# Optimization experiments

Measured on AMD Instinct MI355X. Metric: run time of the kernel, lower is better.

## Reference

```python
import jax, jax.numpy as jnp
import numpy as np

NUM_HEADS = 16
NEG_INF = -9000000000000000.0


def setup_inputs() -> dict:
    key = jax.random.key(0)
    ks = jax.random.split(key, 4)
    B, S, D = 2, 2048, 1024
    x = jax.random.normal(ks[0], (B, S, D), dtype=jnp.float32)
    mask = jax.random.randint(ks[1], (1, 1, S, S), 0, 2, dtype=jnp.int32)
    # xavier-uniform-ish init scaled down for stability
    w_qkv = jax.random.normal(ks[2], (3 * D, D), dtype=jnp.float32) * (1.0 / np.sqrt(D))
    b_qkv = jnp.zeros((3 * D,), dtype=jnp.float32)
    w_o = jax.random.normal(ks[3], (D, D), dtype=jnp.float32) * (1.0 / np.sqrt(D))
    b_o = jnp.zeros((D,), dtype=jnp.float32)
    return {"x": x, "mask": mask, "w_qkv": w_qkv, "b_qkv": b_qkv, "w_o": w_o, "b_o": b_o}


def reference(x, mask, w_qkv, b_qkv, w_o, b_o):
    B, S, D = x.shape
    H = NUM_HEADS
    hd = D // H
    # qkv projection: torch Linear is x @ W.T + b
    qkv = x @ w_qkv.T + b_qkv                      # [B, S, 3D]
    qkv = qkv.reshape(B, S, H, 3 * hd).transpose(0, 2, 1, 3)  # [B, H, S, 3hd]
    q, k, v = jnp.split(qkv, 3, axis=-1)           # each [B, H, S, hd]
    scale = 1.0 / np.sqrt(hd).astype(np.float32)
    logits = jnp.einsum("bhqd,bhkd->bhqk", q, k) * scale  # [B, H, S, S]
    logits = jnp.where(mask == 0, NEG_INF, logits)
    attn = jax.nn.softmax(logits, axis=-1)
    ctx = jnp.einsum("bhqk,bhkd->bhqd", attn, v)   # [B, H, S, hd]
    ctx = ctx.transpose(0, 2, 1, 3).reshape(B, S, D)
    return ctx @ w_o.T + b_o
```

## Files before the change

kernel.cpp:

```cpp
#include <hip/hip_runtime.h>

typedef __attribute__((ext_vector_type(8))) short short8;
typedef __attribute__((ext_vector_type(4))) float f32x4;

#define MFMA16(a, b, c) __builtin_amdgcn_mfma_f32_16x16x32_bf16(a, b, c, 0, 0, 0)

#define BATCH 2
#define SEQ 2048
#define DMODEL 1024
#define NHEADS 16
#define HDIM 64
#define MROWS (BATCH * SEQ)
#define N_QKV (3 * DMODEL)

#define QSCALE 0.1803368801111184f

#define GLDS16(gp, lp)                                                       \
  __builtin_amdgcn_global_load_lds(                                          \
      (const __attribute__((address_space(1))) void*)(gp),                   \
      (__attribute__((address_space(3))) void*)(lp), 16, 0, 0)

#define CFENCE() asm volatile("" ::: "memory")

static __device__ __forceinline__ unsigned short f2bf(float f) {
  unsigned int u = __float_as_uint(f);
  u = (u + 0x7fff + ((u >> 16) & 1)) >> 16;
  return (unsigned short)u;
}

static __device__ __forceinline__ unsigned int pk2bf(float lo, float hi) {
  unsigned int r;
  asm("v_cvt_pk_bf16_f32 %0, %1, %2" : "=v"(r) : "v"(lo), "v"(hi));
  return r;
}

static __device__ __forceinline__ float fexp2(float x) {
  float r;
  asm("v_exp_f32 %0, %1" : "=v"(r) : "v"(x));
  return r;
}

__global__ void prep_kernel(const int* __restrict__ mask,
                            unsigned int* __restrict__ bits,
                            const float* __restrict__ a, unsigned short* __restrict__ oa,
                            int na4, const float* __restrict__ b,
                            unsigned short* __restrict__ ob, int nb4,
                            const float* __restrict__ c,
                            unsigned short* __restrict__ oc, int nc4) {
  if (blockIdx.x < (SEQ * SEQ) / 256) {
    int i = blockIdx.x * 256 + threadIdx.x;
    unsigned long long bl = __ballot(mask[i] != 0);
    if ((threadIdx.x & 63) == 0)
      ((unsigned long long*)bits)[i >> 6] = bl;
    return;
  }
  int j = (blockIdx.x - (SEQ * SEQ) / 256) * 256 + threadIdx.x;
  const float* src;
  unsigned short* dst;
  if (j < na4) {
    src = a; dst = oa;
  } else if ((j -= na4) < nb4) {
    src = b; dst = ob;
  } else if ((j -= nb4) < nc4) {
    src = c; dst = oc;
  } else
    return;
  f32x4 v = ((const f32x4*)src)[j];
  ushort4 o;
  o.x = f2bf(v[0]); o.y = f2bf(v[1]); o.z = f2bf(v[2]); o.w = f2bf(v[3]);
  ((ushort4*)dst)[j] = o;
}

template <int EPI, int BM>
__global__ __launch_bounds__(256, 4) void gemm_bt(
    const unsigned short* __restrict__ A, const unsigned short* __restrict__ Bm,
    const float* __restrict__ bias, int Kdim, int Ndim,
    unsigned short* __restrict__ qb, unsigned short* __restrict__ kb,
    unsigned short* __restrict__ vtb, float* __restrict__ Cout) {
  constexpr int WM = (BM == 128) ? 64 : 32;
  constexpr int NI = WM / 16;
  __shared__ __align__(16) unsigned short lA[2][BM * 32];
  __shared__ __align__(16) unsigned short lB[2][128 * 32];

  int t = threadIdx.x;
  int nwg = gridDim.x * gridDim.y;
  int lin = blockIdx.y * gridDim.x + blockIdx.x;
  int swb = (lin & 7) * (nwg >> 3) + (lin >> 3);
  int m0 = (swb / gridDim.x) * BM, n0 = (swb % gridDim.x) * 128;

  int w = t >> 6, lane = t & 63, quad = lane >> 4, l16 = lane & 15;
  int wm = (w >> 1) * WM, wn = (w & 1) * 64;

  f32x4 acc[NI][4];
#pragma unroll
  for (int i = 0; i < NI; ++i)
#pragma unroll
    for (int j = 0; j < 4; ++j) acc[i][j] = (f32x4){0.f, 0.f, 0.f, 0.f};

  int nK = Kdim >> 5;

#define GSTAGE(buf, kk)                                                      \
  do {                                                                       \
    _Pragma("unroll")                                                        \
    for (int c = 0; c < BM / 64; ++c) {                                      \
      int id = t + c * 256;                                                  \
      int row = id >> 2;                                                     \
      int gc = ((id & 3) ^ (row & 3)) << 3; \
      GLDS16(&A[(size_t)(m0 + row) * Kdim + ((kk) << 5) + gc],               \
             (char*)lA[buf] + (id & ~63) * 16);                              \
    }                                                                        \
    _Pragma("unroll")                                                        \
    for (int c = 0; c < 2; ++c) {                                            \
      int id = t + c * 256;                                                  \
      int row = id >> 2;                                                     \
      int gc = ((id & 3) ^ (row & 3)) << 3;                                  \
      GLDS16(&Bm[(size_t)(n0 + row) * Kdim + ((kk) << 5) + gc],              \
             (char*)lB[buf] + (id & ~63) * 16);                              \
    }                                                                        \
  } while (0)

  GSTAGE(0, 0);
  for (int kk = 0; kk < nK; ++kk) {
    int cur = kk & 1;
    if (kk + 1 < nK) {
      GSTAGE(cur ^ 1, kk + 1);
      if (BM == 128)
        asm volatile("s_waitcnt vmcnt(4)" ::: "memory");
      else
        asm volatile("s_waitcnt vmcnt(3)" ::: "memory");
    } else {
      asm volatile("s_waitcnt vmcnt(0)" ::: "memory");
    }
    __builtin_amdgcn_s_barrier();
    CFENCE();
    __builtin_amdgcn_sched_barrier(0);

    short8 af[NI], bfr[4];
    int rswz = (l16 & 3) << 4;
#pragma unroll
    for (int i = 0; i < NI; ++i)
      af[i] = *(const short8*)((const char*)&lA[cur][(wm + i * 16 + l16) * 32] +
                               ((quad * 16) ^ rswz));
#pragma unroll
    for (int j = 0; j < 4; ++j)
      bfr[j] = *(const short8*)((const char*)&lB[cur][(wn + j * 16 + l16) * 32] +
                                ((quad * 16) ^ rswz));
#pragma unroll
    for (int i = 0; i < NI; ++i)
#pragma unroll
      for (int j = 0; j < 4; ++j) acc[i][j] = MFMA16(af[i], bfr[j], acc[i][j]);

    asm volatile("s_waitcnt lgkmcnt(0)" ::: "memory");
    __builtin_amdgcn_s_barrier();
    CFENCE();
  }

#pragma unroll
  for (int j = 0; j < 4; ++j) {
    int n = n0 + wn + j * 16 + l16;
    float bs = bias[n];
#pragma unroll
    for (int i = 0; i < NI; ++i) {
#pragma unroll
      for (int r = 0; r < 4; ++r) {
        int m = m0 + wm + i * 16 + quad * 4 + r;
        float v = acc[i][j][r] + bs;
        if (EPI == 0) {
          int b = m >> 11, s = m & 2047;
          int h = n / 192, rr = n % 192;
          int bh = (b << 4) + h;
          if (rr < 64)
            qb[((size_t)bh * SEQ + s) * HDIM + rr] = f2bf(v * QSCALE);
          else if (rr < 128)
            kb[((size_t)bh * SEQ + s) * HDIM + (rr - 64)] = f2bf(v);
          else
            vtb[((size_t)bh * HDIM + (rr - 128)) * SEQ + s] = f2bf(v);
        } else {
          Cout[(size_t)m * Ndim + n] = v;
        }
      }
    }
  }
}

__global__ __launch_bounds__(256, 2) void attn_kernel(
    const unsigned short* __restrict__ qbuf, const unsigned short* __restrict__ kbuf,
    const unsigned short* __restrict__ vtbuf, const unsigned int* __restrict__ mbits,
    unsigned short* __restrict__ ctx) {
  __shared__ __align__(16) unsigned short lK[2][64 * 64];
  __shared__ __align__(16) unsigned short lV[2][64 * 64];
  __shared__ __align__(16) unsigned short lP[128 * 64];

  int lin = blockIdx.y * gridDim.x + blockIdx.x;
  int slin = (lin & 7) * 64 + (lin >> 3);
  int qt = slin & 15, bh = slin >> 4;
  int q0 = qt * 128;
  const unsigned short* Q = qbuf + (size_t)bh * SEQ * HDIM;
  const unsigned short* K = kbuf + (size_t)bh * SEQ * HDIM;
  const unsigned short* VT = vtbuf + (size_t)bh * HDIM * SEQ;

  int t = threadIdx.x;
  int w = t >> 6, lane = t & 63, quad = lane >> 4, l16 = lane & 15;
  int swz = (l16 & 7) << 4;

  int qr0 = q0 + w * 32 + l16;
  short8 qf[2][2];
#pragma unroll
  for (int mt = 0; mt < 2; ++mt)
#pragma unroll
    for (int kh = 0; kh < 2; ++kh)
      qf[mt][kh] =
          *(const short8*)&Q[(size_t)(qr0 + mt * 16) * HDIM + kh * 32 + quad * 8];

  const short one = (short)0x3F80;
  short8 ones = {one, one, one, one, one, one, one, one};

  f32x4 o[2][4];
#pragma unroll
  for (int mt = 0; mt < 2; ++mt)
#pragma unroll
    for (int jt = 0; jt < 4; ++jt) o[mt][jt] = (f32x4){0.f, 0.f, 0.f, 0.f};
  f32x4 li4[2];
  li4[0] = (f32x4){0.f, 0.f, 0.f, 0.f};
  li4[1] = (f32x4){0.f, 0.f, 0.f, 0.f};

  int scol = ((lane & 7) ^ (lane >> 3)) << 3;
  const unsigned short* gK = K + (size_t)(w * 8 + (lane >> 3)) * HDIM + scol;
  const unsigned short* gV = VT + (size_t)(w * 8 + (lane >> 3)) * SEQ + scol;

#define STAGE_KV(buf)                                            \
  do {                                                           \
    GLDS16(gK, &lK[buf][(w * 8) * 64]);                          \
    GLDS16(gK + 32 * HDIM, &lK[buf][(32 + w * 8) * 64]);         \
    GLDS16(gV, &lV[buf][(w * 8) * 64]);                          \
    GLDS16(gV + 32 * SEQ, &lV[buf][(32 + w * 8) * 64]);          \
  } while (0)

  STAGE_KV(0);
  gK += 64 * HDIM;
  gV += 64;

  const unsigned int* mrow0 = mbits + (size_t)qr0 * 64;
  const unsigned int* mrow1 = mbits + (size_t)(qr0 + 16) * 64;
  unsigned short* lPr0 = &lP[(w * 32 + l16) * 64];
  unsigned short* lPr1 = &lP[(w * 32 + 16 + l16) * 64];

  for (int it = 0; it < SEQ / 64; ++it) {
    __syncthreads();
    if (it + 1 < SEQ / 64) {
      STAGE_KV((it + 1) & 1);
      gK += 64 * HDIM;
      gV += 64;
    }
    const unsigned short* cK = lK[it & 1];
    const unsigned short* cV = lV[it & 1];

    uint2 mw0 = *(const uint2*)&mrow0[it * 2];
    uint2 mw1 = *(const uint2*)&mrow1[it * 2];

    f32x4 s[2][4];
    __builtin_amdgcn_s_setprio(1);
#pragma unroll
    for (int j = 0; j < 4; ++j) {
      const char* kr = (const char*)&cK[(j * 16 + l16) * 64];
      short8 ka = *(const short8*)(kr + ((quad * 16) ^ swz));
      short8 kc = *(const short8*)(kr + ((64 + quad * 16) ^ swz));
#pragma unroll
      for (int mt = 0; mt < 2; ++mt) {
        f32x4 z = (f32x4){0.f, 0.f, 0.f, 0.f};
        z = MFMA16(ka, qf[mt][0], z);
        z = MFMA16(kc, qf[mt][1], z);
        s[mt][j] = z;
      }
    }
    __builtin_amdgcn_s_setprio(0);

#pragma unroll
    for (int mt = 0; mt < 2; ++mt) {
      unsigned int ma = (mt ? mw1.x : mw0.x) >> (quad * 4);
      unsigned int mb = (mt ? mw1.y : mw0.y) >> (quad * 4);
#pragma unroll
      for (int j = 0; j < 4; ++j) {
        unsigned int sel = (j < 2) ? ma : mb;
        int sh = (j & 1) << 4;
#pragma unroll
        for (int r = 0; r < 4; ++r) {
          float v = (sel & (1u << (sh + r))) ? s[mt][j][r] : -1e30f;
          s[mt][j][r] = fexp2(v);
        }
      }
    }

#pragma unroll
    for (int j = 0; j < 4; ++j) {
      uint2 u0, u1;
      u0.x = pk2bf(s[0][j][0], s[0][j][1]);
      u0.y = pk2bf(s[0][j][2], s[0][j][3]);
      u1.x = pk2bf(s[1][j][0], s[1][j][1]);
      u1.y = pk2bf(s[1][j][2], s[1][j][3]);
      *(uint2*)((char*)lPr0 + ((j * 32 + quad * 8) ^ swz)) = u0;
      *(uint2*)((char*)lPr1 + ((j * 32 + quad * 8) ^ swz)) = u1;
    }

    __builtin_amdgcn_s_setprio(1);
#pragma unroll
    for (int kh = 0; kh < 2; ++kh) {
      short8 pf0 = *(const short8*)((const char*)lPr0 + ((kh * 64 + quad * 16) ^ swz));
      short8 pf1 = *(const short8*)((const char*)lPr1 + ((kh * 64 + quad * 16) ^ swz));
      li4[0] = MFMA16(ones, pf0, li4[0]);
      li4[1] = MFMA16(ones, pf1, li4[1]);
#pragma unroll
      for (int jt = 0; jt < 4; ++jt) {
        const char* vr = (const char*)&cV[(jt * 16 + l16) * 64];
        short8 vf = *(const short8*)(vr + ((kh * 64 + quad * 16) ^ swz));
        o[0][jt] = MFMA16(vf, pf0, o[0][jt]);
        o[1][jt] = MFMA16(vf, pf1, o[1][jt]);
      }
    }
    __builtin_amdgcn_s_setprio(0);
  }

  int b = bh >> 4, h = bh & 15;
#pragma unroll
  for (int mt = 0; mt < 2; ++mt) {
    float inv = 1.0f / li4[mt][0];
    unsigned short* crow =
        ctx + ((size_t)(b * SEQ + qr0 + mt * 16)) * DMODEL + h * HDIM;
#pragma unroll
    for (int jt = 0; jt < 4; ++jt) {
      uint2 u;
      u.x = pk2bf(o[mt][jt][0] * inv, o[mt][jt][1] * inv);
      u.y = pk2bf(o[mt][jt][2] * inv, o[mt][jt][3] * inv);
      *(uint2*)&crow[jt * 16 + quad * 4] = u;
    }
  }
}

extern "C" void kernel_launch(void* const* d_in, const int* in_sizes, int n_in,
                              void* d_out, int out_size, void* d_ws, size_t ws_size,
                              hipStream_t stream) {
  const float* x = (const float*)d_in[0];
  const int* mask = (const int*)d_in[1];
  const float* w_qkv = (const float*)d_in[2];
  const float* b_qkv = (const float*)d_in[3];
  const float* w_o = (const float*)d_in[4];
  const float* b_o = (const float*)d_in[5];
  float* out = (float*)d_out;

  char* ws = (char*)d_ws;
  unsigned short* xb = (unsigned short*)(ws);
  unsigned short* wqkvb = (unsigned short*)(ws + (8ull << 20));
  unsigned short* wob = (unsigned short*)(ws + (14ull << 20));
  unsigned short* qb = (unsigned short*)(ws + (16ull << 20));
  unsigned short* kb = (unsigned short*)(ws + (24ull << 20));
  unsigned short* vtb = (unsigned short*)(ws + (32ull << 20));
  unsigned short* ctx = (unsigned short*)(ws + (40ull << 20));
  unsigned int* mbits = (unsigned int*)(ws + (48ull << 20));

  const int na4 = (MROWS * DMODEL) / 4;
  const int nb4 = (N_QKV * DMODEL) / 4;
  const int nc4 = (DMODEL * DMODEL) / 4;
  const int nmask = (SEQ * SEQ) / 256;
  const int ncvt = (na4 + nb4 + nc4 + 255) / 256;
  prep_kernel<<<nmask + ncvt, 256, 0, stream>>>(mask, mbits, x, xb, na4,
                                                w_qkv, wqkvb, nb4, w_o, wob, nc4);

  gemm_bt<0, 128><<<dim3(N_QKV / 128, MROWS / 128), 256, 0, stream>>>(
      xb, wqkvb, b_qkv, DMODEL, N_QKV, qb, kb, vtb, nullptr);

  attn_kernel<<<dim3(SEQ / 128, BATCH * NHEADS), 256, 0, stream>>>(
      qb, kb, vtb, mbits, ctx);

  gemm_bt<1, 64><<<dim3(DMODEL / 128, MROWS / 64), 256, 0, stream>>>(
      ctx, wob, b_o, DMODEL, DMODEL, nullptr, nullptr, nullptr, out);
}
```

Measured before the change: 216.9 us.

## Halve attention block size, vectorize V-transpose epilogue stores, prefetch mask bits

The attention kernel now uses 128-thread blocks covering 64 query rows instead of 256 threads over 128 rows. That doubles the grid, and each wave stages twice as many K/V rows per tile. The QKV GEMM epilogue hoists the head/column math and writes the transposed V rows as one 4-element vector store instead of four scalar stores. Mask words for the next iteration are loaded one step ahead to hide their latency. Smaller blocks add grid parallelism and cut LDS per block, but each K/V tile is now loaded by more blocks, so K/V global traffic rises.

```diff
diff --git a/kernel.cpp b/kernel.cpp
--- a/kernel.cpp
+++ b/kernel.cpp
@@ -159,42 +159,52 @@
   for (int j = 0; j < 4; ++j) {
     int n = n0 + wn + j * 16 + l16;
     float bs = bias[n];
+    int h = n / 192, rr = n % 192;
 #pragma unroll
     for (int i = 0; i < NI; ++i) {
-#pragma unroll
-      for (int r = 0; r < 4; ++r) {
-        int m = m0 + wm + i * 16 + quad * 4 + r;
-        float v = acc[i][j][r] + bs;
-        if (EPI == 0) {
-          int b = m >> 11, s = m & 2047;
-          int h = n / 192, rr = n % 192;
-          int bh = (b << 4) + h;
-          if (rr < 64)
-            qb[((size_t)bh * SEQ + s) * HDIM + rr] = f2bf(v * QSCALE);
-          else if (rr < 128)
-            kb[((size_t)bh * SEQ + s) * HDIM + (rr - 64)] = f2bf(v);
-          else
-            vtb[((size_t)bh * HDIM + (rr - 128)) * SEQ + s] = f2bf(v);
+      int mb_ = m0 + wm + i * 16 + quad * 4;
+      if (EPI == 0) {
+        int b = mb_ >> 11, s = mb_ & 2047;
+        int bh = (b << 4) + h;
+        if (rr < 64) {
+#pragma unroll
+          for (int r = 0; r < 4; ++r)
+            qb[((size_t)bh * SEQ + s + r) * HDIM + rr] =
+                f2bf((acc[i][j][r] + bs) * QSCALE);
+        } else if (rr < 128) {
+#pragma unroll
+          for (int r = 0; r < 4; ++r)
+            kb[((size_t)bh * SEQ + s + r) * HDIM + (rr - 64)] =
+                f2bf(acc[i][j][r] + bs);
         } else {
-          Cout[(size_t)m * Ndim + n] = v;
+          ushort4 u;
+          u.x = f2bf(acc[i][j][0] + bs);
+          u.y = f2bf(acc[i][j][1] + bs);
+          u.z = f2bf(acc[i][j][2] + bs);
+          u.w = f2bf(acc[i][j][3] + bs);
+          *(ushort4*)&vtb[((size_t)bh * HDIM + (rr - 128)) * SEQ + s] = u;
         }
+      } else {
+#pragma unroll
+        for (int r = 0; r < 4; ++r)
+          Cout[(size_t)(mb_ + r) * Ndim + n] = acc[i][j][r] + bs;
       }
     }
   }
 }
 
-__global__ __launch_bounds__(256, 2) void attn_kernel(
+__global__ __launch_bounds__(128, 2) void attn_kernel(
     const unsigned short* __restrict__ qbuf, const unsigned short* __restrict__ kbuf,
     const unsigned short* __restrict__ vtbuf, const unsigned int* __restrict__ mbits,
     unsigned short* __restrict__ ctx) {
   __shared__ __align__(16) unsigned short lK[2][64 * 64];
   __shared__ __align__(16) unsigned short lV[2][64 * 64];
-  __shared__ __align__(16) unsigned short lP[128 * 64];
+  __shared__ __align__(16) unsigned short lP[64 * 64];
 
   int lin = blockIdx.y * gridDim.x + blockIdx.x;
-  int slin = (lin & 7) * 64 + (lin >> 3);
-  int qt = slin & 15, bh = slin >> 4;
-  int q0 = qt * 128;
+  int slin = (lin & 7) * 128 + (lin >> 3);
+  int qt = slin & 31, bh = slin >> 5;
+  int q0 = qt * 64;
   const unsigned short* Q = qbuf + (size_t)bh * SEQ * HDIM;
   const unsigned short* K = kbuf + (size_t)bh * SEQ * HDIM;
   const unsigned short* VT = vtbuf + (size_t)bh * HDIM * SEQ;
@@ -225,15 +235,19 @@
   li4[1] = (f32x4){0.f, 0.f, 0.f, 0.f};
 
   int scol = ((lane & 7) ^ (lane >> 3)) << 3;
-  const unsigned short* gK = K + (size_t)(w * 8 + (lane >> 3)) * HDIM + scol;
-  const unsigned short* gV = VT + (size_t)(w * 8 + (lane >> 3)) * SEQ + scol;
+  const unsigned short* gK = K + (size_t)(w * 16 + (lane >> 3)) * HDIM + scol;
+  const unsigned short* gV = VT + (size_t)(w * 16 + (lane >> 3)) * SEQ + scol;
 
 #define STAGE_KV(buf)                                            \
   do {                                                           \
-    GLDS16(gK, &lK[buf][(w * 8) * 64]);                          \
-    GLDS16(gK + 32 * HDIM, &lK[buf][(32 + w * 8) * 64]);         \
-    GLDS16(gV, &lV[buf][(w * 8) * 64]);                          \
-    GLDS16(gV + 32 * SEQ, &lV[buf][(32 + w * 8) * 64]);          \
+    GLDS16(gK, &lK[buf][(w * 16) * 64]);                         \
+    GLDS16(gK + 8 * HDIM, &lK[buf][(w * 16 + 8) * 64]);          \
+    GLDS16(gK + 32 * HDIM, &lK[buf][(w * 16 + 32) * 64]);        \
+    GLDS16(gK + 40 * HDIM, &lK[buf][(w * 16 + 40) * 64]);        \
+    GLDS16(gV, &lV[buf][(w * 16) * 64]);                         \
+    GLDS16(gV + 8 * SEQ, &lV[buf][(w * 16 + 8) * 64]);           \
+    GLDS16(gV + 32 * SEQ, &lV[buf][(w * 16 + 32) * 64]);         \
+    GLDS16(gV + 40 * SEQ, &lV[buf][(w * 16 + 40) * 64]);         \
   } while (0)
 
   STAGE_KV(0);
@@ -245,18 +259,21 @@
   unsigned short* lPr0 = &lP[(w * 32 + l16) * 64];
   unsigned short* lPr1 = &lP[(w * 32 + 16 + l16) * 64];
 
+  uint2 mw0 = *(const uint2*)&mrow0[0];
+  uint2 mw1 = *(const uint2*)&mrow1[0];
+
   for (int it = 0; it < SEQ / 64; ++it) {
     __syncthreads();
+    uint2 nmw0, nmw1;
     if (it + 1 < SEQ / 64) {
       STAGE_KV((it + 1) & 1);
       gK += 64 * HDIM;
       gV += 64;
+      nmw0 = *(const uint2*)&mrow0[(it + 1) * 2];
+      nmw1 = *(const uint2*)&mrow1[(it + 1) * 2];
     }
     const unsigned short* cK = lK[it & 1];
     const unsigned short* cV = lV[it & 1];
-
-    uint2 mw0 = *(const uint2*)&mrow0[it * 2];
-    uint2 mw1 = *(const uint2*)&mrow1[it * 2];
 
     f32x4 s[2][4];
     __builtin_amdgcn_s_setprio(1);
@@ -290,6 +307,8 @@
         }
       }
     }
+    mw0 = nmw0;
+    mw1 = nmw1;
 
 #pragma unroll
     for (int j = 0; j < 4; ++j) {
@@ -368,7 +387,7 @@
   gemm_bt<0, 128><<<dim3(N_QKV / 128, MROWS / 128), 256, 0, stream>>>(
       xb, wqkvb, b_qkv, DMODEL, N_QKV, qb, kb, vtb, nullptr);
 
-  attn_kernel<<<dim3(SEQ / 128, BATCH * NHEADS), 256, 0, stream>>>(
+  attn_kernel<<<dim3(SEQ / 64, BATCH * NHEADS), 128, 0, stream>>>(
       qb, kb, vtb, mbits, ctx);
 
   gemm_bt<1, 64><<<dim3(DMODEL / 128, MROWS / 64), 256, 0, stream>>>(
```

Result: no change. 215.7 us (-0.6%).

## Triple-buffer GEMM global-to-LDS pipeline and vectorize V-transpose epilogue stores

Applied to the files above, without the earlier changes.

The GEMM mainloop goes from two LDS stages to three, issuing loads two K-steps ahead with adjusted vmcnt waits, to hide more global latency. Launch bounds drop from 4 to 3 waves per SIMD to fit the larger LDS footprint. The epilogue hoists per-column head math out of the inner loop and writes the transposed V output as 8-byte ushort4 stores instead of four scalar stores. The extra stage raises LDS use per block, which may lower occupancy.

```diff
diff --git a/kernel.cpp b/kernel.cpp
--- a/kernel.cpp
+++ b/kernel.cpp
@@ -72,15 +72,15 @@
 }
 
 template <int EPI, int BM>
-__global__ __launch_bounds__(256, 4) void gemm_bt(
+__global__ __launch_bounds__(256, 3) void gemm_bt(
     const unsigned short* __restrict__ A, const unsigned short* __restrict__ Bm,
     const float* __restrict__ bias, int Kdim, int Ndim,
     unsigned short* __restrict__ qb, unsigned short* __restrict__ kb,
     unsigned short* __restrict__ vtb, float* __restrict__ Cout) {
   constexpr int WM = (BM == 128) ? 64 : 32;
   constexpr int NI = WM / 16;
-  __shared__ __align__(16) unsigned short lA[2][BM * 32];
-  __shared__ __align__(16) unsigned short lB[2][128 * 32];
+  __shared__ __align__(16) unsigned short lA[3][BM * 32];
+  __shared__ __align__(16) unsigned short lB[3][128 * 32];
 
   int t = threadIdx.x;
   int nwg = gridDim.x * gridDim.y;
@@ -120,10 +120,18 @@
   } while (0)
 
   GSTAGE(0, 0);
+  GSTAGE(1, 1);
+  int stage = 2;
   for (int kk = 0; kk < nK; ++kk) {
-    int cur = kk & 1;
-    if (kk + 1 < nK) {
-      GSTAGE(cur ^ 1, kk + 1);
+    int cur = kk % 3;
+    if (kk + 2 < nK) {
+      GSTAGE(stage, kk + 2);
+      stage = (stage + 1) % 3;
+      if (BM == 128)
+        asm volatile("s_waitcnt vmcnt(8)" ::: "memory");
+      else
+        asm volatile("s_waitcnt vmcnt(6)" ::: "memory");
+    } else if (kk + 1 < nK) {
       if (BM == 128)
         asm volatile("s_waitcnt vmcnt(4)" ::: "memory");
       else
@@ -159,25 +167,35 @@
   for (int j = 0; j < 4; ++j) {
     int n = n0 + wn + j * 16 + l16;
     float bs = bias[n];
+    int h = n / 192, rr = n % 192;
 #pragma unroll
     for (int i = 0; i < NI; ++i) {
-#pragma unroll
-      for (int r = 0; r < 4; ++r) {
-        int m = m0 + wm + i * 16 + quad * 4 + r;
-        float v = acc[i][j][r] + bs;
-        if (EPI == 0) {
-          int b = m >> 11, s = m & 2047;
-          int h = n / 192, rr = n % 192;
-          int bh = (b << 4) + h;
-          if (rr < 64)
-            qb[((size_t)bh * SEQ + s) * HDIM + rr] = f2bf(v * QSCALE);
-          else if (rr < 128)
-            kb[((size_t)bh * SEQ + s) * HDIM + (rr - 64)] = f2bf(v);
-          else
-            vtb[((size_t)bh * HDIM + (rr - 128)) * SEQ + s] = f2bf(v);
+      int mb_ = m0 + wm + i * 16 + quad * 4;
+      if (EPI == 0) {
+        int b = mb_ >> 11, s = mb_ & 2047;
+        int bh = (b << 4) + h;
+        if (rr < 64) {
+#pragma unroll
+          for (int r = 0; r < 4; ++r)
+            qb[((size_t)bh * SEQ + s + r) * HDIM + rr] =
+                f2bf((acc[i][j][r] + bs) * QSCALE);
+        } else if (rr < 128) {
+#pragma unroll
+          for (int r = 0; r < 4; ++r)
+            kb[((size_t)bh * SEQ + s + r) * HDIM + (rr - 64)] =
+                f2bf(acc[i][j][r] + bs);
         } else {
-          Cout[(size_t)m * Ndim + n] = v;
+          ushort4 u;
+          u.x = f2bf(acc[i][j][0] + bs);
+          u.y = f2bf(acc[i][j][1] + bs);
+          u.z = f2bf(acc[i][j][2] + bs);
+          u.w = f2bf(acc[i][j][3] + bs);
+          *(ushort4*)&vtb[((size_t)bh * HDIM + (rr - 128)) * SEQ + s] = u;
         }
+      } else {
+#pragma unroll
+        for (int r = 0; r < 4; ++r)
+          Cout[(size_t)(mb_ + r) * Ndim + n] = acc[i][j][r] + bs;
       }
     }
   }
```

Measured after the change: 213.7 us. No clear change (-1.5%).
